# Kernel tuning notes

Hardware: AMD Instinct MI355X
Metric: run time of the kernel (lower is better)

The kernel has to match this reference:

```python
import jax, jax.numpy as jnp
import numpy as np

NUM_NODES = 200000
NUM_EDGES = 4000000
NUM_GRAPHS = 512
D = 20
OUT = 5


def setup_inputs() -> dict:
    key = jax.random.key(0)
    k1, k2, k3, k4, k5, k6, k7 = jax.random.split(key, 7)
    x = jax.random.normal(k1, (NUM_NODES, D), dtype=jnp.float32)
    edge_index = jax.random.randint(k2, (2, NUM_EDGES), 0, NUM_NODES, dtype=jnp.int64)
    batch = jnp.sort(jax.random.randint(k3, (NUM_NODES,), 0, NUM_GRAPHS, dtype=jnp.int64))
    # GCNConv weight (glorot-ish) and bias; Linear(20 -> 5) weight/bias
    W1 = jax.random.normal(k4, (D, D), dtype=jnp.float32) / np.sqrt(D)
    b1 = jnp.zeros((D,), dtype=jnp.float32)
    W_out = jax.random.normal(k5, (D, OUT), dtype=jnp.float32) / np.sqrt(D)
    b_out = jax.random.normal(k6, (OUT,), dtype=jnp.float32) * 0.01
    return {"x": x, "edge_index": edge_index, "batch": batch,
            "W1": W1, "b1": b1, "W_out": W_out, "b_out": b_out}


def gcn_conv(x, edge_index, W, b, num_nodes):
    # PyG GCNConv: add self-loops, symmetric norm, linear transform, scatter-add, bias
    loop = jnp.arange(num_nodes, dtype=edge_index.dtype)
    src = jnp.concatenate([edge_index[0], loop])
    dst = jnp.concatenate([edge_index[1], loop])
    deg = jax.ops.segment_sum(jnp.ones_like(dst, dtype=x.dtype), dst, num_segments=num_nodes)
    dinv = jnp.where(deg > 0, jax.lax.rsqrt(deg), 0.0)
    norm = dinv[src] * dinv[dst]  # [E+N]
    h = x @ W                      # [N, D] transform first (cheaper than per-edge)
    msg = h[src] * norm[:, None]   # gather + scale  [E+N, D]
    out = jax.ops.segment_sum(msg, dst, num_segments=num_nodes)  # scatter-add
    return out + b


def reference(x, edge_index, batch, W1, b1, W_out, b_out):
    h = gcn_conv(x, edge_index, W1, b1, NUM_NODES)
    h = jax.nn.relu(h)
    # global mean pool per graph
    sums = jax.ops.segment_sum(h, batch, num_segments=NUM_GRAPHS)          # [G, D]
    cnts = jax.ops.segment_sum(jnp.ones((h.shape[0],), h.dtype), batch, num_segments=NUM_GRAPHS)
    pooled = sums / jnp.maximum(cnts, 1.0)[:, None]
    logits = pooled @ W_out + b_out                                        # [G, 5]
    return jax.nn.softmax(logits, axis=-1)
```

## Files before the change

kernel.cpp:

```cpp
#include <hip/hip_runtime.h>
#include <hip/hip_fp16.h>

#define N_NODES 200000
#define N_EDGES 4000000
#define N_GRAPHS 512
#define D 20
#define OUT 5

#define BSH 6
#define BN 64
#define NB 3125
#define NBP 3128
#define NBB 3129
#define NC 500
#define CHUNK 8000
#define MAX_EB 1792
#define GMAX 8

__launch_bounds__(1024)
__global__ void k_hist(const int* __restrict__ dst, int* __restrict__ hist_g,
                       float* __restrict__ gsum) {
    __shared__ int h[NBP];
    int t = threadIdx.x;
    if (blockIdx.x == 0) {
        for (int j = t; j < N_GRAPHS * D; j += 1024) gsum[j] = 0.f;
    }
    for (int j = t; j < NBP; j += 1024) h[j] = 0;
    __syncthreads();
    int base = blockIdx.x * CHUNK;
    for (int k = t; k < CHUNK; k += 1024) atomicAdd(&h[dst[base + k] >> BSH], 1);
    __syncthreads();
    for (int j = t; j < NBP; j += 1024) hist_g[blockIdx.x * NBP + j] = h[j];
}

__launch_bounds__(512)
__global__ void k_scan_col(int* __restrict__ hist_g, int* __restrict__ tot_g) {
    __shared__ int4 s[512];
    int t = threadIdx.x;
    int b0 = blockIdx.x * 4;
    int4 v = make_int4(0, 0, 0, 0);
    if (t < NC) v = *(const int4*)&hist_g[t * NBP + b0];
    s[t] = v;
    __syncthreads();
    for (int off = 1; off < 512; off <<= 1) {
        int4 a = make_int4(0, 0, 0, 0);
        if (t >= off) a = s[t - off];
        __syncthreads();
        s[t].x += a.x; s[t].y += a.y; s[t].z += a.z; s[t].w += a.w;
        __syncthreads();
    }
    if (t < NC) {
        int4 ex = s[t];
        ex.x -= v.x; ex.y -= v.y; ex.z -= v.z; ex.w -= v.w;
        *(int4*)&hist_g[t * NBP + b0] = ex;
    }
    if (t == 511) *(int4*)&tot_g[b0] = s[511];
}

__launch_bounds__(1024)
__global__ void k_scan_tot(const int* __restrict__ tot_g, int* __restrict__ bucket_base) {
    __shared__ int ps[1024];
    int t = threadIdx.x;
    int base = t * 4;
    int loc[4];
    int sum = 0;
    #pragma unroll
    for (int j = 0; j < 4; j++) {
        int idx = base + j;
        int x = (idx < NBP) ? tot_g[idx] : 0;
        loc[j] = sum;
        sum += x;
    }
    ps[t] = sum;
    __syncthreads();
    for (int off = 1; off < 1024; off <<= 1) {
        int a = (t >= off) ? ps[t - off] : 0;
        __syncthreads();
        ps[t] += a;
        __syncthreads();
    }
    int carry = (t > 0) ? ps[t - 1] : 0;
    #pragma unroll
    for (int j = 0; j < 4; j++) {
        int idx = base + j;
        if (idx < NBB) bucket_base[idx] = carry + loc[j];
    }
}

__launch_bounds__(1024)
__global__ void k_partition(const int* __restrict__ src, const int* __restrict__ dst,
                            const int* __restrict__ hist_g, const int* __restrict__ bucket_base,
                            int* __restrict__ ebuf) {
    __shared__ int cur[NBP];
    int t = threadIdx.x, c = blockIdx.x;
    for (int j = t; j < NBP; j += 1024) cur[j] = hist_g[c * NBP + j] + bucket_base[j];
    __syncthreads();
    int base = c * CHUNK;
    for (int k = t; k < CHUNK; k += 1024) {
        int d = dst[base + k];
        int sv = src[base + k];
        int b = d >> BSH;
        int pos = atomicAdd(&cur[b], 1);
        ebuf[pos] = (sv << BSH) | (d & (BN - 1));
    }
}

__launch_bounds__(256)
__global__ void k_count_xh(const int* __restrict__ ebuf, const int* __restrict__ bucket_base,
                           const float4* __restrict__ x4, int* __restrict__ offs_g,
                           uint2* __restrict__ xh2) {
    __shared__ int cnt[BN];
    __shared__ int s[BN];
    __shared__ float sdi[BN];
    int b = blockIdx.x, t = threadIdx.x;
    int eb = bucket_base[b], ee = bucket_base[b + 1];
    if (t < BN) cnt[t] = 0;
    __syncthreads();
    for (int k = eb + t; k < ee; k += 256) atomicAdd(&cnt[ebuf[k] & (BN - 1)], 1);
    __syncthreads();
    int nbn = N_NODES - (b << BSH); if (nbn > BN) nbn = BN;
    int v = (t < BN) ? cnt[t] : 0;
    if (t < BN) s[t] = v;
    __syncthreads();
    for (int off = 1; off < BN; off <<= 1) {
        int a = 0;
        if (t < BN && t >= off) a = s[t - off];
        __syncthreads();
        if (t < BN) s[t] += a;
        __syncthreads();
    }
    if (t < nbn) {
        int node = (b << BSH) + t;
        offs_g[node] = eb + s[t] - v;
        sdi[t] = rsqrtf((float)(v + 1));
    }
    __syncthreads();
    int nw = nbn * 5;
    for (int j = t; j < nw; j += 256) {
        int vl = j / 5, q = j - vl * 5;
        int node = (b << BSH) + vl;
        float4 xv = x4[node * 5 + q];
        float di = sdi[vl];
        __half2 h0 = __float22half2_rn(make_float2(xv.x * di, xv.y * di));
        __half2 h1 = __float22half2_rn(make_float2(xv.z * di, xv.w * di));
        uint2 u;
        u.x = *(unsigned int*)&h0;
        u.y = *(unsigned int*)&h1;
        xh2[node * 5 + q] = u;
    }
}

__launch_bounds__(256, 8)
__global__ void k_gather_fused(const int* __restrict__ ebuf, const int* __restrict__ bucket_base,
                               const int* __restrict__ offs_g, const uint2* __restrict__ xh2,
                               const int* __restrict__ batch, const float* __restrict__ W1,
                               const float* __restrict__ b1, float* __restrict__ gsum) {
    __shared__ int loff[BN + 1];
    __shared__ int cur[BN];
    __shared__ int lcsr[MAX_EB];
    __shared__ float w[D * D];
    __shared__ float wb[D];
    __shared__ float sagg[BN][21];
    __shared__ float lgsum[GMAX][D];
    int b = blockIdx.x, t = threadIdx.x;
    int eb = bucket_base[b], ee = bucket_base[b + 1];
    int n = ee - eb;
    int nbn = N_NODES - (b << BSH); if (nbn > BN) nbn = BN;

    for (int j = t; j < D * D; j += 256) w[j] = W1[j];
    if (t < D) wb[t] = b1[t];
    if (t < GMAX * D) ((float*)lgsum)[t] = 0.f;
    if (t < nbn) {
        int o = offs_g[(b << BSH) + t] - eb;
        loff[t] = o;
        cur[t] = o;
    }
    if (t == 0) loff[nbn] = n;
    __syncthreads();

    for (int k = t; k < n; k += 256) {
        int p = ebuf[eb + k];
        int pos = atomicAdd(&cur[p & (BN - 1)], 1);
        if (pos < MAX_EB) lcsr[pos] = p >> BSH;
    }
    __syncthreads();

    int nw = nbn * 5;
    for (int j = t; j < nw; j += 256) {
        int vl = j / 5, q = j - vl * 5;
        int node = (b << BSH) + vl;
        uint2 u = xh2[node * 5 + q];
        float2 a0 = __half22float2(*(__half2*)&u.x);
        float2 a1 = __half22float2(*(__half2*)&u.y);
        float accx = a0.x, accy = a0.y, accz = a1.x, accw = a1.y;
        float bccx = 0.f, bccy = 0.f, bccz = 0.f, bccw = 0.f;
        int lo = loff[vl], hi = loff[vl + 1];
        if (hi > MAX_EB) hi = MAX_EB;
        if (lo > MAX_EB) lo = MAX_EB;
        int k = lo;
        for (; k + 8 <= hi; k += 8) {
            int s0 = lcsr[k],     s1 = lcsr[k + 1], s2 = lcsr[k + 2], s3 = lcsr[k + 3];
            int s4 = lcsr[k + 4], s5 = lcsr[k + 5], s6 = lcsr[k + 6], s7 = lcsr[k + 7];
            uint2 m0 = xh2[s0 * 5 + q];
            uint2 m1 = xh2[s1 * 5 + q];
            uint2 m2 = xh2[s2 * 5 + q];
            uint2 m3 = xh2[s3 * 5 + q];
            uint2 m4 = xh2[s4 * 5 + q];
            uint2 m5 = xh2[s5 * 5 + q];
            uint2 m6 = xh2[s6 * 5 + q];
            uint2 m7 = xh2[s7 * 5 + q];
            float2 p0 = __half22float2(*(__half2*)&m0.x);
            float2 p1 = __half22float2(*(__half2*)&m0.y);
            float2 q0 = __half22float2(*(__half2*)&m1.x);
            float2 q1 = __half22float2(*(__half2*)&m1.y);
            float2 r0 = __half22float2(*(__half2*)&m2.x);
            float2 r1 = __half22float2(*(__half2*)&m2.y);
            float2 t0 = __half22float2(*(__half2*)&m3.x);
            float2 t1 = __half22float2(*(__half2*)&m3.y);
            accx += p0.x + q0.x; accy += p0.y + q0.y;
            accz += p1.x + q1.x; accw += p1.y + q1.y;
            bccx += r0.x + t0.x; bccy += r0.y + t0.y;
            bccz += r1.x + t1.x; bccw += r1.y + t1.y;
            float2 p2 = __half22float2(*(__half2*)&m4.x);
            float2 p3 = __half22float2(*(__half2*)&m4.y);
            float2 q2 = __half22float2(*(__half2*)&m5.x);
            float2 q3 = __half22float2(*(__half2*)&m5.y);
            float2 r2 = __half22float2(*(__half2*)&m6.x);
            float2 r3 = __half22float2(*(__half2*)&m6.y);
            float2 t2 = __half22float2(*(__half2*)&m7.x);
            float2 t3 = __half22float2(*(__half2*)&m7.y);
            accx += p2.x + q2.x; accy += p2.y + q2.y;
            accz += p3.x + q3.x; accw += p3.y + q3.y;
            bccx += r2.x + t2.x; bccy += r2.y + t2.y;
            bccz += r3.x + t3.x; bccw += r3.y + t3.y;
        }
        for (; k + 4 <= hi; k += 4) {
            int s0 = lcsr[k], s1 = lcsr[k + 1], s2 = lcsr[k + 2], s3 = lcsr[k + 3];
            uint2 m0 = xh2[s0 * 5 + q];
            uint2 m1 = xh2[s1 * 5 + q];
            uint2 m2 = xh2[s2 * 5 + q];
            uint2 m3 = xh2[s3 * 5 + q];
            float2 p0 = __half22float2(*(__half2*)&m0.x);
            float2 p1 = __half22float2(*(__half2*)&m0.y);
            float2 q0 = __half22float2(*(__half2*)&m1.x);
            float2 q1 = __half22float2(*(__half2*)&m1.y);
            float2 r0 = __half22float2(*(__half2*)&m2.x);
            float2 r1 = __half22float2(*(__half2*)&m2.y);
            float2 t0 = __half22float2(*(__half2*)&m3.x);
            float2 t1 = __half22float2(*(__half2*)&m3.y);
            accx += p0.x + q0.x; accy += p0.y + q0.y;
            accz += p1.x + q1.x; accw += p1.y + q1.y;
            bccx += r0.x + t0.x; bccy += r0.y + t0.y;
            bccz += r1.x + t1.x; bccw += r1.y + t1.y;
        }
        for (; k < hi; k++) {
            int sv = lcsr[k];
            uint2 m = xh2[sv * 5 + q];
            float2 m0 = __half22float2(*(__half2*)&m.x);
            float2 m1 = __half22float2(*(__half2*)&m.y);
            accx += m0.x; accy += m0.y; accz += m1.x; accw += m1.y;
        }
        sagg[vl][q * 4 + 0] = accx + bccx;
        sagg[vl][q * 4 + 1] = accy + bccy;
        sagg[vl][q * 4 + 2] = accz + bccz;
        sagg[vl][q * 4 + 3] = accw + bccw;
    }
    __syncthreads();

    int g0 = batch[b << BSH];
    int glast = batch[(b << BSH) + nbn - 1];
    int gcnt = glast - g0 + 1;

    if (t < nbn) {
        int node = (b << BSH) + t;
        float di = rsqrtf((float)(loff[t + 1] - loff[t] + 1));
        int gi = batch[node] - g0;
        float pre[D];
        #pragma unroll
        for (int d = 0; d < D; d++) pre[d] = sagg[t][d];
        int t20 = t % D;
        bool fits = (gcnt <= GMAX);
        for (int jj = 0; jj < D; jj++) {
            int o = t20 + jj; if (o >= D) o -= D;
            float h = 0.f;
            #pragma unroll
            for (int d = 0; d < D; d++) h = fmaf(pre[d], w[d * D + o], h);
            h = fmaf(h, di, wb[o]);
            h = fmaxf(h, 0.f);
            if (fits) atomicAdd(&lgsum[gi][o], h);
            else atomicAdd(&gsum[(g0 + gi) * D + o], h);
        }
    }
    __syncthreads();
    if (gcnt <= GMAX && t < gcnt * D) {
        atomicAdd(&gsum[(g0 + t / D) * D + (t % D)], lgsum[t / D][t % D]);
    }
}

__launch_bounds__(64)
__global__ void k_head(const float* __restrict__ gsum, const int* __restrict__ batch,
                       const float* __restrict__ W_out, const float* __restrict__ b_out,
                       float* __restrict__ out) {
    __shared__ float wo[D * OUT];
    __shared__ float bo[OUT];
    int t = threadIdx.x;
    for (int j = t; j < D * OUT; j += 64) wo[j] = W_out[j];
    if (t < OUT) bo[t] = b_out[t];
    __syncthreads();
    int g = blockIdx.x * 64 + t;
    if (g >= N_GRAPHS) return;
    auto lb = [&](int key) {
        int lo = 0, hi = N_NODES;
        while (lo < hi) { int mid = (lo + hi) >> 1; if (batch[mid] < key) lo = mid + 1; else hi = mid; }
        return lo;
    };
    int cnt = lb(g + 1) - lb(g);
    float inv = 1.0f / fmaxf((float)cnt, 1.0f);
    float logits[OUT];
    #pragma unroll
    for (int o = 0; o < OUT; o++) logits[o] = bo[o];
    #pragma unroll
    for (int d = 0; d < D; d++) {
        float p = gsum[g * D + d] * inv;
        #pragma unroll
        for (int o = 0; o < OUT; o++) logits[o] = fmaf(p, wo[d * OUT + o], logits[o]);
    }
    float m = logits[0];
    #pragma unroll
    for (int o = 1; o < OUT; o++) m = fmaxf(m, logits[o]);
    float ex[OUT], sum = 0.f;
    #pragma unroll
    for (int o = 0; o < OUT; o++) { ex[o] = __expf(logits[o] - m); sum += ex[o]; }
    float isum = 1.0f / sum;
    #pragma unroll
    for (int o = 0; o < OUT; o++) out[g * OUT + o] = ex[o] * isum;
}

extern "C" void kernel_launch(void* const* d_in, const int* in_sizes, int n_in,
                              void* d_out, int out_size, void* d_ws, size_t ws_size,
                              hipStream_t stream) {
    const float* x     = (const float*)d_in[0];
    const int*   edge  = (const int*)d_in[1];
    const int*   batch = (const int*)d_in[2];
    const float* W1    = (const float*)d_in[3];
    const float* b1    = (const float*)d_in[4];
    const float* W_out = (const float*)d_in[5];
    const float* b_out = (const float*)d_in[6];
    float* out = (float*)d_out;

    const int* src = edge;
    const int* dst = edge + N_EDGES;
    char* ws = (char*)d_ws;

    int*   hist_g      = (int*)(ws);
    int*   tot_g       = (int*)(ws + 6256000);
    int*   bucket_base = (int*)(ws + 6268544);
    float* gsum        = (float*)(ws + 6281152);
    int*   offs_g      = (int*)(ws + 6322176);
    uint2* xh2         = (uint2*)(ws + 7122176);
    int*   ebuf        = (int*)(ws + 15122176);

    k_hist<<<NC, 1024, 0, stream>>>(dst, hist_g, gsum);
    k_scan_col<<<NBP / 4, 512, 0, stream>>>(hist_g, tot_g);
    k_scan_tot<<<1, 1024, 0, stream>>>(tot_g, bucket_base);
    k_partition<<<NC, 1024, 0, stream>>>(src, dst, hist_g, bucket_base, ebuf);
    k_count_xh<<<NB, 256, 0, stream>>>(ebuf, bucket_base, (const float4*)x, offs_g, xh2);
    k_gather_fused<<<NB, 256, 0, stream>>>(ebuf, bucket_base, offs_g, xh2, batch, W1, b1, gsum);
    k_head<<<(N_GRAPHS + 63) / 64, 64, 0, stream>>>(gsum, batch, W_out, b_out, out);
}
```

Measured before the change: 174.1 us.

## Replace single-pass bucket partition with two-level coarse/fine radix partition

The single scatter into 3125 fine buckets is replaced by two passes. The first scatters edges into 49 coarse buckets, with cursors claimed through global atomics. The second splits each coarse bucket into its 64 fine buckets using per-block histograms and atomic cursors. The per-column prefix scan of the chunk histograms becomes a plain column sum accumulated with atomics. The aim is to make the scatter writes more local and to remove the 500-row scan, at the cost of an extra read and write pass over the edge buffer and edge order that now depends on scheduling.

```diff
diff --git a/kernel.cpp b/kernel.cpp
--- a/kernel.cpp
+++ b/kernel.cpp
@@ -9,56 +9,47 @@
 
 #define BSH 6
 #define BN 64
-#define NB 3125
-#define NBP 3128
+#define NFB 3125
+#define NFBP 3136
 #define NBB 3129
+#define NCB 49
 #define NC 500
 #define CHUNK 8000
+#define CH2 7168
+#define NCH2 13
 #define MAX_EB 1792
 #define GMAX 8
 
 __launch_bounds__(1024)
 __global__ void k_hist(const int* __restrict__ dst, int* __restrict__ hist_g,
-                       float* __restrict__ gsum) {
-    __shared__ int h[NBP];
+                       float* __restrict__ gsum, int* __restrict__ bucket_tot) {
+    __shared__ int h[NFBP];
     int t = threadIdx.x;
     if (blockIdx.x == 0) {
         for (int j = t; j < N_GRAPHS * D; j += 1024) gsum[j] = 0.f;
-    }
-    for (int j = t; j < NBP; j += 1024) h[j] = 0;
+        for (int j = t; j < NFBP; j += 1024) bucket_tot[j] = 0;
+    }
+    for (int j = t; j < NFBP; j += 1024) h[j] = 0;
     __syncthreads();
     int base = blockIdx.x * CHUNK;
     for (int k = t; k < CHUNK; k += 1024) atomicAdd(&h[dst[base + k] >> BSH], 1);
     __syncthreads();
-    for (int j = t; j < NBP; j += 1024) hist_g[blockIdx.x * NBP + j] = h[j];
-}
-
-__launch_bounds__(512)
-__global__ void k_scan_col(int* __restrict__ hist_g, int* __restrict__ tot_g) {
-    __shared__ int4 s[512];
-    int t = threadIdx.x;
-    int b0 = blockIdx.x * 4;
-    int4 v = make_int4(0, 0, 0, 0);
-    if (t < NC) v = *(const int4*)&hist_g[t * NBP + b0];
-    s[t] = v;
-    __syncthreads();
-    for (int off = 1; off < 512; off <<= 1) {
-        int4 a = make_int4(0, 0, 0, 0);
-        if (t >= off) a = s[t - off];
-        __syncthreads();
-        s[t].x += a.x; s[t].y += a.y; s[t].z += a.z; s[t].w += a.w;
-        __syncthreads();
-    }
-    if (t < NC) {
-        int4 ex = s[t];
-        ex.x -= v.x; ex.y -= v.y; ex.z -= v.z; ex.w -= v.w;
-        *(int4*)&hist_g[t * NBP + b0] = ex;
-    }
-    if (t == 511) *(int4*)&tot_g[b0] = s[511];
+    for (int j = t; j < NFBP; j += 1024) hist_g[blockIdx.x * NFBP + j] = h[j];
+}
+
+__launch_bounds__(256)
+__global__ void k_colsum(const int* __restrict__ hist_g, int* __restrict__ bucket_tot) {
+    int col = blockIdx.x * 256 + threadIdx.x;
+    if (col >= NFBP) return;
+    int r0 = blockIdx.y * 50;
+    int sum = 0;
+    for (int r = r0; r < r0 + 50; r++) sum += hist_g[r * NFBP + col];
+    if (sum) atomicAdd(&bucket_tot[col], sum);
 }
 
 __launch_bounds__(1024)
-__global__ void k_scan_tot(const int* __restrict__ tot_g, int* __restrict__ bucket_base) {
+__global__ void k_scan_tot(const int* __restrict__ bucket_tot, int* __restrict__ bucket_base,
+                           int* __restrict__ fcursor, int* __restrict__ ccursorA) {
     __shared__ int ps[1024];
     int t = threadIdx.x;
     int base = t * 4;
@@ -67,7 +58,7 @@
     #pragma unroll
     for (int j = 0; j < 4; j++) {
         int idx = base + j;
-        int x = (idx < NBP) ? tot_g[idx] : 0;
+        int x = (idx < NFBP) ? bucket_tot[idx] : 0;
         loc[j] = sum;
         sum += x;
     }
@@ -83,25 +74,61 @@
     #pragma unroll
     for (int j = 0; j < 4; j++) {
         int idx = base + j;
-        if (idx < NBB) bucket_base[idx] = carry + loc[j];
-    }
+        if (idx < NFBP) {
+            int v = carry + loc[j];
+            bucket_base[idx] = v;
+            fcursor[idx] = v;
+        }
+    }
+    __syncthreads();
+    if (t < NCB) ccursorA[t] = bucket_base[t << 6];
 }
 
 __launch_bounds__(1024)
-__global__ void k_partition(const int* __restrict__ src, const int* __restrict__ dst,
-                            const int* __restrict__ hist_g, const int* __restrict__ bucket_base,
-                            int* __restrict__ ebuf) {
-    __shared__ int cur[NBP];
+__global__ void k_partA(const int* __restrict__ src, const int* __restrict__ dst,
+                        int* __restrict__ ccursorA, int* __restrict__ ebufA) {
+    __shared__ int h[NCB];
+    __shared__ int lcur[NCB];
     int t = threadIdx.x, c = blockIdx.x;
-    for (int j = t; j < NBP; j += 1024) cur[j] = hist_g[c * NBP + j] + bucket_base[j];
+    if (t < NCB) h[t] = 0;
     __syncthreads();
     int base = c * CHUNK;
+    for (int k = t; k < CHUNK; k += 1024) atomicAdd(&h[dst[base + k] >> 12], 1);
+    __syncthreads();
+    if (t < NCB) lcur[t] = atomicAdd(&ccursorA[t], h[t]);
+    __syncthreads();
     for (int k = t; k < CHUNK; k += 1024) {
         int d = dst[base + k];
         int sv = src[base + k];
-        int b = d >> BSH;
-        int pos = atomicAdd(&cur[b], 1);
-        ebuf[pos] = (sv << BSH) | (d & (BN - 1));
+        int cb = d >> 12;
+        int pos = atomicAdd(&lcur[cb], 1);
+        ebufA[pos] = (sv << 12) | (d & 4095);
+    }
+}
+
+__launch_bounds__(1024)
+__global__ void k_partB(const int* __restrict__ ebufA, const int* __restrict__ bucket_base,
+                        int* __restrict__ fcursor, int* __restrict__ ebuf) {
+    int cb = blockIdx.x, j = blockIdx.y, t = threadIdx.x;
+    int cbase = bucket_base[cb << 6];
+    int cend_idx = (cb + 1) << 6; if (cend_idx > NFB) cend_idx = NFB;
+    int cend = bucket_base[cend_idx];
+    int lo = cbase + j * CH2;
+    int hi = lo + CH2; if (hi > cend) hi = cend;
+    if (lo >= hi) return;
+    __shared__ int h[64];
+    __shared__ int lcur[64];
+    if (t < 64) h[t] = 0;
+    __syncthreads();
+    for (int k = lo + t; k < hi; k += 1024) atomicAdd(&h[(ebufA[k] >> 6) & 63], 1);
+    __syncthreads();
+    if (t < 64) lcur[t] = atomicAdd(&fcursor[(cb << 6) + t], h[t]);
+    __syncthreads();
+    for (int k = lo + t; k < hi; k += 1024) {
+        int p = ebufA[k];
+        int sb = (p >> 6) & 63;
+        int pos = atomicAdd(&lcur[sb], 1);
+        ebuf[pos] = ((p >> 12) << 6) | (p & 63);
     }
 }
 
@@ -353,18 +380,22 @@
     char* ws = (char*)d_ws;
 
     int*   hist_g      = (int*)(ws);
-    int*   tot_g       = (int*)(ws + 6256000);
-    int*   bucket_base = (int*)(ws + 6268544);
-    float* gsum        = (float*)(ws + 6281152);
-    int*   offs_g      = (int*)(ws + 6322176);
-    uint2* xh2         = (uint2*)(ws + 7122176);
-    int*   ebuf        = (int*)(ws + 15122176);
-
-    k_hist<<<NC, 1024, 0, stream>>>(dst, hist_g, gsum);
-    k_scan_col<<<NBP / 4, 512, 0, stream>>>(hist_g, tot_g);
-    k_scan_tot<<<1, 1024, 0, stream>>>(tot_g, bucket_base);
-    k_partition<<<NC, 1024, 0, stream>>>(src, dst, hist_g, bucket_base, ebuf);
-    k_count_xh<<<NB, 256, 0, stream>>>(ebuf, bucket_base, (const float4*)x, offs_g, xh2);
-    k_gather_fused<<<NB, 256, 0, stream>>>(ebuf, bucket_base, offs_g, xh2, batch, W1, b1, gsum);
+    int*   bucket_tot  = (int*)(ws + 6272000);
+    int*   bucket_base = (int*)(ws + 6284544);
+    int*   fcursor     = (int*)(ws + 6297088);
+    int*   ccursorA    = (int*)(ws + 6309632);
+    float* gsum        = (float*)(ws + 6309888);
+    int*   offs_g      = (int*)(ws + 6350848);
+    uint2* xh2         = (uint2*)(ws + 7150848);
+    int*   ebufA       = (int*)(ws + 15150848);
+    int*   ebuf        = (int*)(ws + 31150848);
+
+    k_hist<<<NC, 1024, 0, stream>>>(dst, hist_g, gsum, bucket_tot);
+    k_colsum<<<dim3(13, 10), 256, 0, stream>>>(hist_g, bucket_tot);
+    k_scan_tot<<<1, 1024, 0, stream>>>(bucket_tot, bucket_base, fcursor, ccursorA);
+    k_partA<<<NC, 1024, 0, stream>>>(src, dst, ccursorA, ebufA);
+    k_partB<<<dim3(NCB, NCH2), 1024, 0, stream>>>(ebufA, bucket_base, fcursor, ebuf);
+    k_count_xh<<<NFB, 256, 0, stream>>>(ebuf, bucket_base, (const float4*)x, offs_g, xh2);
+    k_gather_fused<<<NFB, 256, 0, stream>>>(ebuf, bucket_base, offs_g, xh2, batch, W1, b1, gsum);
     k_head<<<(N_GRAPHS + 63) / 64, 64, 0, stream>>>(gsum, batch, W_out, b_out, out);
 }
```

Result: faster. 153.2 us (-12.0%).
